# Kernel tuning notes

Measured on AMD Instinct MI355X. Metric: run time of the kernel, lower is better.

## Reference

```python
import jax, jax.numpy as jnp
import numpy as np

B, T, D = 4, 4096, 512
H, L = 8, 6
HD = D // H
BS = 64          # block_size
MLP = 2048
VOCAB = 96000
MAX_SCALE = 10000.0
LN_EPS = 1e-6


def _sinusoidal_pe(length, dim, max_scale=MAX_SCALE):
    # flax common_layers sinusoidal init (concat sin|cos halves)
    pos = np.arange(length)[:, None].astype(np.float32)
    div = np.exp(np.arange(0, dim, 2).astype(np.float32) * -(np.log(max_scale) / dim))
    pe = np.zeros((length, dim), dtype=np.float32)
    pe[:, : dim // 2] = np.sin(pos * div)
    pe[:, dim // 2:] = np.cos(pos * div)
    return jnp.asarray(pe)

_PE = _sinusoidal_pe(T, D)


def layer_norm(x, scale, bias):
    m = jnp.mean(x, axis=-1, keepdims=True)
    v = jnp.mean(jnp.square(x - m), axis=-1, keepdims=True)
    return (x - m) * jax.lax.rsqrt(v + LN_EPS) * scale + bias


def local_block_attention(x, mask, wq, wk, wv, wo, stagger):
    # x: [B, T, D], mask: [B, T] bool (True = real token)
    b, t, d = x.shape
    if stagger:
        lp = BS // 2
        rp = BS - lp
        x = jnp.pad(x, ((0, 0), (lp, rp), (0, 0)))
        mask = jnp.pad(mask, ((0, 0), (lp, rp)))
    tp = x.shape[1]
    nb = tp // BS
    xb = x.reshape(b, nb, BS, d)          # [B, nb, BS, D]
    mb = mask.reshape(b, nb, BS)          # [B, nb, BS]
    scale = 1.0 / float(np.sqrt(HD))
    q = jnp.einsum('bnsd,dhf->bnshf', xb, wq) * scale
    k = jnp.einsum('bnsd,dhf->bnshf', xb, wk)
    v = jnp.einsum('bnsd,dhf->bnshf', xb, wv)
    scores = jnp.einsum('bnqhf,bnkhf->bnhqk', q, k)       # [B, nb, H, BS, BS]
    scores = jnp.where(mb[:, :, None, None, :], scores, jnp.asarray(-1e9, scores.dtype))
    probs = jax.nn.softmax(scores, axis=-1)
    o = jnp.einsum('bnhqk,bnkhf->bnqhf', probs, v)
    o = jnp.einsum('bnqhf,hfd->bnqd', o, wo).reshape(b, tp, d)
    if stagger:
        o = o[:, lp:lp + t]
    return o


def setup_inputs() -> dict:
    key = jax.random.key(0)
    ks = jax.random.split(key, 10)
    inputs = jax.random.randint(ks[0], (B, T), 0, VOCAB)
    embed = jax.random.normal(ks[1], (VOCAB, D), dtype=jnp.float32)
    s = 0.02
    wq = jax.random.normal(ks[2], (L, D, H, HD), dtype=jnp.float32) * s
    wk = jax.random.normal(ks[3], (L, D, H, HD), dtype=jnp.float32) * s
    wv = jax.random.normal(ks[4], (L, D, H, HD), dtype=jnp.float32) * s
    wo = jax.random.normal(ks[5], (L, H, HD, D), dtype=jnp.float32) * s
    w1 = jax.random.normal(ks[6], (L, D, MLP), dtype=jnp.float32) * s
    b1 = jnp.zeros((L, MLP), dtype=jnp.float32)
    w2 = jax.random.normal(ks[7], (L, MLP, D), dtype=jnp.float32) * s
    b2 = jnp.zeros((L, D), dtype=jnp.float32)
    ln1_s = jnp.ones((L, D), dtype=jnp.float32)
    ln1_b = jnp.zeros((L, D), dtype=jnp.float32)
    ln2_s = jnp.ones((L, D), dtype=jnp.float32)
    ln2_b = jnp.zeros((L, D), dtype=jnp.float32)
    lnf_s = jnp.ones((D,), dtype=jnp.float32)
    lnf_b = jnp.zeros((D,), dtype=jnp.float32)
    return {'inputs': inputs, 'embed': embed, 'wq': wq, 'wk': wk, 'wv': wv, 'wo': wo,
            'ln1_s': ln1_s, 'ln1_b': ln1_b, 'ln2_s': ln2_s, 'ln2_b': ln2_b,
            'w1': w1, 'b1': b1, 'w2': w2, 'b2': b2, 'lnf_s': lnf_s, 'lnf_b': lnf_b}


def reference(inputs, embed, wq, wk, wv, wo, ln1_s, ln1_b, ln2_s, ln2_b,
              w1, b1, w2, b2, lnf_s, lnf_b):
    mask = inputs > 0                      # src padding mask [B, T]
    x = embed[inputs.astype(jnp.int32)]    # [B, T, D]
    x = x + _PE[None, :, :]                # sinusoidal position embedding
    for lyr in range(L):
        stagger = (lyr % 2 == 1)           # stagger_local_blocks on odd layers
        h = layer_norm(x, ln1_s[lyr], ln1_b[lyr])
        h = local_block_attention(h, mask, wq[lyr], wk[lyr], wv[lyr], wo[lyr], stagger)
        x = x + h
        y = layer_norm(x, ln2_s[lyr], ln2_b[lyr])
        y = jnp.matmul(jax.nn.relu(jnp.matmul(y, w1[lyr]) + b1[lyr]), w2[lyr]) + b2[lyr]
        x = x + y
    return layer_norm(x, lnf_s, lnf_b)
```

## Files before the change

kernel.cpp:

```cpp
#include <hip/hip_runtime.h>

typedef unsigned short u16;
typedef unsigned int   u32;
typedef __attribute__((ext_vector_type(8))) short short8;
typedef __attribute__((ext_vector_type(4))) float f32x4;

#define TSEQ   4096
#define DMODEL 512
#define NHEAD  8
#define HDIM   64
#define NLAYER 6
#define MLPD   2048

#define GPTR(p) (const __attribute__((address_space(1))) void*)(p)
#define LPTR(p) (__attribute__((address_space(3))) void*)(p)

__device__ __forceinline__ u16 f2b(float f) {
  u32 u = __float_as_uint(f);
  u32 r = (u + 0x7fffu + ((u >> 16) & 1u)) >> 16;
  return (u16)r;
}
__device__ __forceinline__ float b2f(u16 h) { return __uint_as_float(((u32)h) << 16); }

__device__ __forceinline__ short8 ld8g(const u16* p, bool ok) {
  if (ok) return *(const short8*)p;
  short8 z = {0, 0, 0, 0, 0, 0, 0, 0};
  return z;
}

__global__ __launch_bounds__(256) void transpose_convert_all(
    const float* __restrict__ wq, const float* __restrict__ wk,
    const float* __restrict__ wv, const float* __restrict__ wo,
    const float* __restrict__ w1, const float* __restrict__ w2,
    u16* __restrict__ wqkv_bt, u16* __restrict__ wo_bt,
    u16* __restrict__ w1_bt, u16* __restrict__ w2_bt) {
  __shared__ float tile[64][65];
  int bx = blockIdx.x, l = blockIdx.y;
  const float* W; u16* out; int K, N, Ntot, ro, kb, nb2;
  if (bx < 256) {
    int which = bx >> 6, local = bx & 63;
    K = 512; N = 512; kb = local & 7; nb2 = local >> 3;
    if (which == 0)      { W = wq; out = wqkv_bt; Ntot = 1536; ro = 0; }
    else if (which == 1) { W = wk; out = wqkv_bt; Ntot = 1536; ro = 512; }
    else if (which == 2) { W = wv; out = wqkv_bt; Ntot = 1536; ro = 1024; }
    else                 { W = wo; out = wo_bt;   Ntot = 512;  ro = 0; }
  } else if (bx < 512) {
    int local = bx - 256;
    W = w1; out = w1_bt; K = 512; N = 2048; Ntot = 2048; ro = 0;
    kb = local & 7; nb2 = local >> 3;
  } else {
    int local = bx - 512;
    W = w2; out = w2_bt; K = 2048; N = 512; Ntot = 512; ro = 0;
    kb = local >> 3; nb2 = local & 7;
  }
  int k0 = kb * 64, n0 = nb2 * 64;
  const float* Wl = W + (size_t)l * K * N;
  u16* Ol = out + (size_t)l * Ntot * K;
  int tx = threadIdx.x & 15, ty = threadIdx.x >> 4;
#pragma unroll
  for (int p = 0; p < 4; ++p) {
    int k = k0 + p * 16 + ty;
    float4 v = *(const float4*)(Wl + (size_t)k * N + n0 + tx * 4);
    tile[p * 16 + ty][tx * 4 + 0] = v.x;
    tile[p * 16 + ty][tx * 4 + 1] = v.y;
    tile[p * 16 + ty][tx * 4 + 2] = v.z;
    tile[p * 16 + ty][tx * 4 + 3] = v.w;
  }
  __syncthreads();
#pragma unroll
  for (int p = 0; p < 4; ++p) {
    int n = n0 + p * 16 + ty;
    ushort4 s;
    s.x = f2b(tile[tx * 4 + 0][p * 16 + ty]);
    s.y = f2b(tile[tx * 4 + 1][p * 16 + ty]);
    s.z = f2b(tile[tx * 4 + 2][p * 16 + ty]);
    s.w = f2b(tile[tx * 4 + 3][p * 16 + ty]);
    *(ushort4*)(Ol + (size_t)(ro + n) * K + k0 + tx * 4) = s;
  }
}

__global__ void embed_pe_kernel(const int* __restrict__ idx,
                                const float* __restrict__ embed,
                                float* __restrict__ x) {
  int i = blockIdx.x;
  int t = i & (TSEQ - 1);
  int tok = idx[i];
  int c = threadIdx.x * 4;
  float4 e = *(const float4*)(embed + (size_t)tok * DMODEL + c);
  float vals[4] = {e.x, e.y, e.z, e.w};
  float o[4];
#pragma unroll
  for (int j = 0; j < 4; ++j) {
    int col = c + j;
    int jj = (col < 256) ? col : col - 256;
    float div = __expf((float)jj * -0.035977892078032f);
    float arg = (float)t * div;
    o[j] = vals[j] + ((col < 256) ? __sinf(arg) : __cosf(arg));
  }
  float4 r = {o[0], o[1], o[2], o[3]};
  *(float4*)(x + (size_t)i * DMODEL + c) = r;
}

template <bool OUT_BF16>
__global__ __launch_bounds__(256) void ln_kernel(
    const float* __restrict__ x, const float* __restrict__ gamma,
    const float* __restrict__ beta, void* __restrict__ out) {
  int wave = threadIdx.x >> 6, lane = threadIdx.x & 63;
  int row = (blockIdx.x << 2) + wave;
  const float* xr = x + (size_t)row * DMODEL + lane * 8;
  float4 a = *(const float4*)xr;
  float4 b = *(const float4*)(xr + 4);
  float v[8] = {a.x, a.y, a.z, a.w, b.x, b.y, b.z, b.w};
  float s = 0.f;
#pragma unroll
  for (int j = 0; j < 8; ++j) s += v[j];
#pragma unroll
  for (int off = 1; off < 64; off <<= 1) s += __shfl_xor(s, off, 64);
  float mean = s * (1.0f / 512.0f);
  float q = 0.f;
#pragma unroll
  for (int j = 0; j < 8; ++j) { float d = v[j] - mean; q += d * d; }
#pragma unroll
  for (int off = 1; off < 64; off <<= 1) q += __shfl_xor(q, off, 64);
  float rstd = rsqrtf(q * (1.0f / 512.0f) + 1e-6f);
  float4 g0 = *(const float4*)(gamma + lane * 8);
  float4 g1 = *(const float4*)(gamma + lane * 8 + 4);
  float4 p0 = *(const float4*)(beta + lane * 8);
  float4 p1 = *(const float4*)(beta + lane * 8 + 4);
  float g[8] = {g0.x, g0.y, g0.z, g0.w, g1.x, g1.y, g1.z, g1.w};
  float be[8] = {p0.x, p0.y, p0.z, p0.w, p1.x, p1.y, p1.z, p1.w};
  float r[8];
#pragma unroll
  for (int j = 0; j < 8; ++j) r[j] = (v[j] - mean) * rstd * g[j] + be[j];
  if (OUT_BF16) {
    uint4 pk;
    pk.x = (u32)f2b(r[0]) | ((u32)f2b(r[1]) << 16);
    pk.y = (u32)f2b(r[2]) | ((u32)f2b(r[3]) << 16);
    pk.z = (u32)f2b(r[4]) | ((u32)f2b(r[5]) << 16);
    pk.w = (u32)f2b(r[6]) | ((u32)f2b(r[7]) << 16);
    *(uint4*)((u16*)out + (size_t)row * DMODEL + lane * 8) = pk;
  } else {
    float4 r0 = {r[0], r[1], r[2], r[3]};
    float4 r1 = {r[4], r[5], r[6], r[7]};
    float* op = (float*)out + (size_t)row * DMODEL + lane * 8;
    *(float4*)op = r0;
    *(float4*)(op + 4) = r1;
  }
}

template <int FLAGS>
__global__ __launch_bounds__(256) void gemm_kernel(
    const u16* __restrict__ A, const u16* __restrict__ Bt,
    const float* __restrict__ bias, const float* __restrict__ resid,
    void* __restrict__ out, void* __restrict__ out2, int M, int N, int K) {
  __shared__ __align__(16) u16 a_lds[3][128][32];
  __shared__ __align__(16) u16 b_lds[3][128][32];
  int m0 = blockIdx.y * 128, n0 = blockIdx.x * 128;
  int t = threadIdx.x;
  int lr = t >> 2, lc = (t & 3) * 8;
  int wave = t >> 6, lane = t & 63;
  int wm = (wave >> 1) * 64, wn = (wave & 1) * 64;
  int fr = lane & 15, quad = lane >> 4;

  f32x4 acc[4][4];
  f32x4 zz = {0.f, 0.f, 0.f, 0.f};
#pragma unroll
  for (int i = 0; i < 4; ++i)
#pragma unroll
    for (int j = 0; j < 4; ++j) acc[i][j] = zz;

  const u16* Ag0 = A + (size_t)(m0 + lr) * K + lc;
  const u16* Ag1 = A + (size_t)(m0 + lr + 64) * K + lc;
  const u16* Bg0 = Bt + (size_t)(n0 + lr) * K + lc;
  const u16* Bg1 = Bt + (size_t)(n0 + lr + 64) * K + lc;

  __builtin_amdgcn_global_load_lds(GPTR(Ag0), LPTR(&a_lds[0][lr][lc]), 16, 0, 0);
  __builtin_amdgcn_global_load_lds(GPTR(Ag1), LPTR(&a_lds[0][lr + 64][lc]), 16, 0, 0);
  __builtin_amdgcn_global_load_lds(GPTR(Bg0), LPTR(&b_lds[0][lr][lc]), 16, 0, 0);
  __builtin_amdgcn_global_load_lds(GPTR(Bg1), LPTR(&b_lds[0][lr + 64][lc]), 16, 0, 0);

  int T = K >> 5;
  int buf = 0;
  for (int tt = 0; tt < T; ++tt) {
    int nb = buf + 1 == 3 ? 0 : buf + 1;
    if (tt + 1 < T) {
      int off = (tt + 1) << 5;
      __builtin_amdgcn_global_load_lds(GPTR(Ag0 + off), LPTR(&a_lds[nb][lr][lc]), 16, 0, 0);
      __builtin_amdgcn_global_load_lds(GPTR(Ag1 + off), LPTR(&a_lds[nb][lr + 64][lc]), 16, 0, 0);
      __builtin_amdgcn_global_load_lds(GPTR(Bg0 + off), LPTR(&b_lds[nb][lr][lc]), 16, 0, 0);
      __builtin_amdgcn_global_load_lds(GPTR(Bg1 + off), LPTR(&b_lds[nb][lr + 64][lc]), 16, 0, 0);
      asm volatile("s_waitcnt vmcnt(4)\n\ts_barrier" ::: "memory");
    } else {
      asm volatile("s_waitcnt vmcnt(0)\n\ts_barrier" ::: "memory");
    }
    short8 af[4], bf[4];
#pragma unroll
    for (int mi = 0; mi < 4; ++mi)
      af[mi] = *(const short8*)&a_lds[buf][wm + mi * 16 + fr][quad * 8];
#pragma unroll
    for (int ni = 0; ni < 4; ++ni)
      bf[ni] = *(const short8*)&b_lds[buf][wn + ni * 16 + fr][quad * 8];
#pragma unroll
    for (int mi = 0; mi < 4; ++mi)
#pragma unroll
      for (int ni = 0; ni < 4; ++ni)
        acc[mi][ni] = __builtin_amdgcn_mfma_f32_16x16x32_bf16(
            af[mi], bf[ni], acc[mi][ni], 0, 0, 0);
    buf = nb;
  }

  if (FLAGS & 16) {
#pragma unroll
    for (int mi = 0; mi < 4; ++mi)
#pragma unroll
      for (int ni = 0; ni < 4; ++ni) {
        int colg = n0 + wn + ni * 16 + fr;
        if (colg < 1024) {
#pragma unroll
          for (int r = 0; r < 4; ++r) {
            int rowg = m0 + wm + mi * 16 + quad * 4 + r;
            ((u16*)out)[(size_t)rowg * 1024 + colg] = f2b(acc[mi][ni][r]);
          }
        } else {
          int hh = (colg - 1024) >> 6, ff = colg & 63;
          int rowg0 = m0 + wm + mi * 16 + quad * 4;
          int bb = rowg0 >> 12, tok = rowg0 & 4095;
          ushort4 pk;
          pk.x = f2b(acc[mi][ni][0]);
          pk.y = f2b(acc[mi][ni][1]);
          pk.z = f2b(acc[mi][ni][2]);
          pk.w = f2b(acc[mi][ni][3]);
          *(ushort4*)((u16*)out2 +
                      ((size_t)(bb * 8 + hh) * 64 + ff) * 4096 + tok) = pk;
        }
      }
    return;
  }

#pragma unroll
  for (int mi = 0; mi < 4; ++mi)
#pragma unroll
    for (int ni = 0; ni < 4; ++ni) {
      int colg = n0 + wn + ni * 16 + fr;
      float bv = (FLAGS & 1) ? bias[colg] : 0.0f;
#pragma unroll
      for (int r = 0; r < 4; ++r) {
        int rowg = m0 + wm + mi * 16 + quad * 4 + r;
        float val = acc[mi][ni][r] + bv;
        if (FLAGS & 2) val = fmaxf(val, 0.0f);
        if (FLAGS & 4) val += resid[(size_t)rowg * N + colg];
        if (FLAGS & 8)
          ((u16*)out)[(size_t)rowg * N + colg] = f2b(val);
        else
          ((float*)out)[(size_t)rowg * N + colg] = val;
      }
    }
}

template <int FLAGS>
__global__ __launch_bounds__(512, 2) void gemm256_kernel(
    const u16* __restrict__ A, const u16* __restrict__ Bt,
    const float* __restrict__ bias, const float* __restrict__ resid,
    void* __restrict__ out, void* __restrict__ out2, int M, int N, int K) {
  __shared__ __align__(16) u16 a_lds[2][16384];
  __shared__ __align__(16) u16 b_lds[2][16384];
  int m0 = blockIdx.y * 256, n0 = blockIdx.x * 256;
  int tid = threadIdx.x;
  int w = tid >> 6, lane = tid & 63;
  int fr = lane & 15, quad = lane >> 4;
  int wms = (w >> 2) * 8;
  int wns = (w & 3) * 4;
  int rS = lane >> 2;
  int cS = ((lane & 3) * 8) ^ ((lane & 32) ? 16 : 0);
  const u16* Asrc = A + (size_t)(m0 + w * 16 + rS) * K + cS;
  const u16* Bsrc = Bt + (size_t)(n0 + w * 16 + rS) * K + cS;
  int wBase = w * 1024 + lane * 8;
  int rdoff = fr * 32 + ((quad * 8) ^ ((fr & 8) ? 16 : 0));
  int NT = K >> 6;

  f32x4 acc[8][4];
  f32x4 zz = {0.f, 0.f, 0.f, 0.f};
#pragma unroll
  for (int i = 0; i < 8; ++i)
#pragma unroll
    for (int j = 0; j < 4; ++j) acc[i][j] = zz;

  auto stage_half = [&](int hh) {
    if (hh >= 4 * NT) return;
    int th = hh >> 2, part = hh & 3, kk = part >> 1;
    const u16* src = (part & 1) ? Bsrc : Asrc;
    u16* ldsb = (part & 1) ? &b_lds[0][0] : &a_lds[0][0];
    ldsb += (size_t)(th & 1) * 16384;
    src += (size_t)th * 64 + kk * 32;
#pragma unroll
    for (int j = 0; j < 2; ++j) {
      __builtin_amdgcn_global_load_lds(GPTR(src + (size_t)j * 128 * K),
                                       LPTR(ldsb + kk * 512 + j * 8192 + wBase),
                                       16, 0, 0);
    }
  };

#pragma unroll
  for (int hh = 0; hh < 6; ++hh) stage_half(hh);
  asm volatile("s_waitcnt vmcnt(4)\n\ts_barrier" ::: "memory");

  for (int t = 0; t < NT; ++t) {
    const u16* ap = a_lds[t & 1];
    const u16* bp = b_lds[t & 1];
    short8 aF[4], bF[4];
#define LDA256(mi_, kk_) (*(const short8*)&ap[((wms + (mi_)) * 2 + (kk_)) * 512 + rdoff])
#define LDB256(ni_, kk_) (*(const short8*)&bp[((wns + (ni_)) * 2 + (kk_)) * 512 + rdoff])
#pragma unroll
    for (int ni = 0; ni < 4; ++ni) bF[ni] = LDB256(ni, 0);
#pragma unroll
    for (int mi = 0; mi < 4; ++mi) aF[mi] = LDA256(mi, 0);
    stage_half(4 * t + 6);
    __builtin_amdgcn_s_barrier();
    __builtin_amdgcn_s_setprio(1);
#pragma unroll
    for (int mi = 0; mi < 4; ++mi)
#pragma unroll
      for (int ni = 0; ni < 4; ++ni)
        acc[mi][ni] = __builtin_amdgcn_mfma_f32_16x16x32_bf16(
            aF[mi], bF[ni], acc[mi][ni], 0, 0, 0);
    __builtin_amdgcn_s_setprio(0);
    __builtin_amdgcn_s_barrier();
#pragma unroll
    for (int mi = 0; mi < 4; ++mi) aF[mi] = LDA256(4 + mi, 0);
    stage_half(4 * t + 7);
    __builtin_amdgcn_s_barrier();
    __builtin_amdgcn_s_setprio(1);
#pragma unroll
    for (int mi = 0; mi < 4; ++mi)
#pragma unroll
      for (int ni = 0; ni < 4; ++ni)
        acc[4 + mi][ni] = __builtin_amdgcn_mfma_f32_16x16x32_bf16(
            aF[mi], bF[ni], acc[4 + mi][ni], 0, 0, 0);
    __builtin_amdgcn_s_setprio(0);
    __builtin_amdgcn_s_barrier();
#pragma unroll
    for (int ni = 0; ni < 4; ++ni) bF[ni] = LDB256(ni, 1);
#pragma unroll
    for (int mi = 0; mi < 4; ++mi) aF[mi] = LDA256(mi, 1);
    stage_half(4 * t + 8);
    __builtin_amdgcn_s_barrier();
    __builtin_amdgcn_s_setprio(1);
#pragma unroll
    for (int mi = 0; mi < 4; ++mi)
#pragma unroll
      for (int ni = 0; ni < 4; ++ni)
        acc[mi][ni] = __builtin_amdgcn_mfma_f32_16x16x32_bf16(
            aF[mi], bF[ni], acc[mi][ni], 0, 0, 0);
    __builtin_amdgcn_s_setprio(0);
    __builtin_amdgcn_s_barrier();
#pragma unroll
    for (int mi = 0; mi < 4; ++mi) aF[mi] = LDA256(4 + mi, 1);
    stage_half(4 * t + 9);
    __builtin_amdgcn_s_barrier();
    __builtin_amdgcn_s_setprio(1);
#pragma unroll
    for (int mi = 0; mi < 4; ++mi)
#pragma unroll
      for (int ni = 0; ni < 4; ++ni)
        acc[4 + mi][ni] = __builtin_amdgcn_mfma_f32_16x16x32_bf16(
            aF[mi], bF[ni], acc[4 + mi][ni], 0, 0, 0);
    __builtin_amdgcn_s_setprio(0);
    if (t + 2 == NT)
      asm volatile("s_waitcnt vmcnt(0)\n\ts_barrier" ::: "memory");
    else if (t + 1 < NT)
      asm volatile("s_waitcnt vmcnt(4)\n\ts_barrier" ::: "memory");
#undef LDA256
#undef LDB256
  }

  int wm = (w >> 2) * 128, wn = (w & 3) * 64;
  if (FLAGS & 16) {
#pragma unroll
    for (int mi = 0; mi < 8; ++mi)
#pragma unroll
      for (int ni = 0; ni < 4; ++ni) {
        int colg = n0 + wn + ni * 16 + fr;
        if (colg < 1024) {
#pragma unroll
          for (int r = 0; r < 4; ++r) {
            int rowg = m0 + wm + mi * 16 + quad * 4 + r;
            ((u16*)out)[(size_t)rowg * 1024 + colg] = f2b(acc[mi][ni][r]);
          }
        } else {
          int hh = (colg - 1024) >> 6, ff = colg & 63;
          int rowg0 = m0 + wm + mi * 16 + quad * 4;
          int bb2 = rowg0 >> 12, tok = rowg0 & 4095;
          ushort4 pk;
          pk.x = f2b(acc[mi][ni][0]);
          pk.y = f2b(acc[mi][ni][1]);
          pk.z = f2b(acc[mi][ni][2]);
          pk.w = f2b(acc[mi][ni][3]);
          *(ushort4*)((u16*)out2 +
                      ((size_t)(bb2 * 8 + hh) * 64 + ff) * 4096 + tok) = pk;
        }
      }
    return;
  }

#pragma unroll
  for (int mi = 0; mi < 8; ++mi)
#pragma unroll
    for (int ni = 0; ni < 4; ++ni) {
      int colg = n0 + wn + ni * 16 + fr;
      float bv = (FLAGS & 1) ? bias[colg] : 0.0f;
#pragma unroll
      for (int r = 0; r < 4; ++r) {
        int rowg = m0 + wm + mi * 16 + quad * 4 + r;
        float val = acc[mi][ni][r] + bv;
        if (FLAGS & 2) val = fmaxf(val, 0.0f);
        if (FLAGS & 4) val += resid[(size_t)rowg * N + colg];
        if (FLAGS & 8)
          ((u16*)out)[(size_t)rowg * N + colg] = f2b(val);
        else
          ((float*)out)[(size_t)rowg * N + colg] = val;
      }
    }
}

__global__ __launch_bounds__(128) void attn_mfma_kernel(
    const u16* __restrict__ qk, const u16* __restrict__ vt,
    const int* __restrict__ tokens, u16* __restrict__ o, int sh) {
  __shared__ __align__(16) u16 ps[2][64][72];
  __shared__ float kmask[64];
  int n = blockIdx.x, hg = blockIdx.y, b = blockIdx.z;
  int tid = threadIdx.x;
  int w = tid >> 6, lane = tid & 63;
  int head = hg * 2 + w;
  int fr = lane & 15, quad = lane >> 4;

  if (tid < 64) {
    int pp = n * 64 + tid - sh;
    kmask[tid] =
        (pp >= 0 && pp < TSEQ && tokens[(size_t)b * TSEQ + pp] > 0) ? 1.f : 0.f;
  }
  __syncthreads();

  const u16* qkb = qk + (size_t)b * TSEQ * 1024;

  f32x4 st[4][4];
  f32x4 zz = {0.f, 0.f, 0.f, 0.f};
#pragma unroll
  for (int i = 0; i < 4; ++i)
#pragma unroll
    for (int j = 0; j < 4; ++j) st[i][j] = zz;
#pragma unroll
  for (int kk = 0; kk < 2; ++kk) {
    short8 ka[4], qb[4];
#pragma unroll
    for (int mi = 0; mi < 4; ++mi) {
      int p = n * 64 + mi * 16 + fr - sh;
      ka[mi] = ld8g(qkb + (ptrdiff_t)p * 1024 + 512 + head * 64 + kk * 32 + quad * 8,
                    p >= 0 && p < TSEQ);
    }
#pragma unroll
    for (int ni = 0; ni < 4; ++ni) {
      int p = n * 64 + ni * 16 + fr - sh;
      qb[ni] = ld8g(qkb + (ptrdiff_t)p * 1024 + head * 64 + kk * 32 + quad * 8,
                    p >= 0 && p < TSEQ);
    }
#pragma unroll
    for (int mi = 0; mi < 4; ++mi)
#pragma unroll
      for (int ni = 0; ni < 4; ++ni)
        st[mi][ni] = __builtin_amdgcn_mfma_f32_16x16x32_bf16(
            ka[mi], qb[ni], st[mi][ni], 0, 0, 0);
  }

  float kmv[4][4];
#pragma unroll
  for (int mi = 0; mi < 4; ++mi)
#pragma unroll
    for (int r = 0; r < 4; ++r) kmv[mi][r] = kmask[mi * 16 + quad * 4 + r];
#pragma unroll
  for (int ni = 0; ni < 4; ++ni) {
    float mx = -3.0e38f;
#pragma unroll
    for (int mi = 0; mi < 4; ++mi)
#pragma unroll
      for (int r = 0; r < 4; ++r) {
        float s = (kmv[mi][r] > 0.f) ? st[mi][ni][r] * 0.125f : -1.0e9f;
        st[mi][ni][r] = s;
        mx = fmaxf(mx, s);
      }
    mx = fmaxf(mx, __shfl_xor(mx, 16, 64));
    mx = fmaxf(mx, __shfl_xor(mx, 32, 64));
    float sm = 0.f;
#pragma unroll
    for (int mi = 0; mi < 4; ++mi)
#pragma unroll
      for (int r = 0; r < 4; ++r) {
        float e = __expf(st[mi][ni][r] - mx);
        st[mi][ni][r] = e;
        sm += e;
      }
    sm += __shfl_xor(sm, 16, 64);
    sm += __shfl_xor(sm, 32, 64);
    float inv = 1.0f / sm;
#pragma unroll
    for (int mi = 0; mi < 4; ++mi)
#pragma unroll
      for (int r = 0; r < 4; ++r) st[mi][ni][r] *= inv;
  }

#pragma unroll
  for (int mi = 0; mi < 4; ++mi)
#pragma unroll
    for (int ni = 0; ni < 4; ++ni) {
      uint2 pk;
      pk.x = (u32)f2b(st[mi][ni][0]) | ((u32)f2b(st[mi][ni][1]) << 16);
      pk.y = (u32)f2b(st[mi][ni][2]) | ((u32)f2b(st[mi][ni][3]) << 16);
      *(uint2*)&ps[w][ni * 16 + fr][mi * 16 + quad * 4] = pk;
    }
  __syncthreads();

  f32x4 oc[4][4];
#pragma unroll
  for (int i = 0; i < 4; ++i)
#pragma unroll
    for (int j = 0; j < 4; ++j) oc[i][j] = zz;
  const u16* vtb = vt + (size_t)(b * 8 + head) * 64 * 4096;
#pragma unroll
  for (int kk = 0; kk < 2; ++kk) {
    short8 pa[4], vb[4];
#pragma unroll
    for (int mi = 0; mi < 4; ++mi)
      pa[mi] = *(const short8*)&ps[w][mi * 16 + fr][kk * 32 + quad * 8];
    int key0 = n * 64 - sh + kk * 32 + quad * 8;
    bool kok = (key0 >= 0) && (key0 < TSEQ);
#pragma unroll
    for (int ni = 0; ni < 4; ++ni)
      vb[ni] = ld8g(vtb + (size_t)(ni * 16 + fr) * 4096 + key0, kok);
#pragma unroll
    for (int mi = 0; mi < 4; ++mi)
#pragma unroll
      for (int ni = 0; ni < 4; ++ni)
        oc[mi][ni] = __builtin_amdgcn_mfma_f32_16x16x32_bf16(
            pa[mi], vb[ni], oc[mi][ni], 0, 0, 0);
  }

#pragma unroll
  for (int mi = 0; mi < 4; ++mi)
#pragma unroll
    for (int ni = 0; ni < 4; ++ni)
#pragma unroll
      for (int r = 0; r < 4; ++r) {
        int q = mi * 16 + quad * 4 + r;
        int p = n * 64 + q - sh;
        if (p >= 0 && p < TSEQ)
          o[((size_t)(b * TSEQ + p)) * DMODEL + head * 64 + ni * 16 + fr] =
              f2b(oc[mi][ni][r]);
      }
}

extern "C" void kernel_launch(void* const* d_in, const int* in_sizes, int n_in,
                              void* d_out, int out_size, void* d_ws, size_t ws_size,
                              hipStream_t stream) {
  (void)in_sizes; (void)n_in; (void)out_size; (void)ws_size;
  const int*   tokens = (const int*)d_in[0];
  const float* embed  = (const float*)d_in[1];
  const float* wq = (const float*)d_in[2];
  const float* wk = (const float*)d_in[3];
  const float* wv = (const float*)d_in[4];
  const float* wo = (const float*)d_in[5];
  const float* ln1_s = (const float*)d_in[6];
  const float* ln1_b = (const float*)d_in[7];
  const float* ln2_s = (const float*)d_in[8];
  const float* ln2_b = (const float*)d_in[9];
  const float* w1 = (const float*)d_in[10];
  const float* b1 = (const float*)d_in[11];
  const float* w2 = (const float*)d_in[12];
  const float* b2 = (const float*)d_in[13];
  const float* lnf_s = (const float*)d_in[14];
  const float* lnf_b = (const float*)d_in[15];

  char* ws = (char*)d_ws;
  const size_t MB = 1024ull * 1024ull;
  float* x     = (float*)(ws + 0);
  u16* h       = (u16*)(ws + 32 * MB);
  u16* qk      = (u16*)(ws + 48 * MB);
  u16* vt      = (u16*)(ws + 82 * MB);
  u16* obuf    = (u16*)(ws + 99 * MB);
  u16* hidden  = (u16*)(ws + 48 * MB);
  u16* wqkv_bt = (u16*)(ws + 116 * MB);
  u16* wo_bt   = (u16*)(ws + 126 * MB);
  u16* w1_bt   = (u16*)(ws + 130 * MB);
  u16* w2_bt   = (u16*)(ws + 143 * MB);

  transpose_convert_all<<<dim3(768, 6), 256, 0, stream>>>(
      wq, wk, wv, wo, w1, w2, wqkv_bt, wo_bt, w1_bt, w2_bt);

  embed_pe_kernel<<<16384, 128, 0, stream>>>(tokens, embed, x);

  for (int l = 0; l < NLAYER; ++l) {
    int sh = (l & 1) ? 32 : 0;
    int nb = (l & 1) ? 65 : 64;
    ln_kernel<true><<<4096, 256, 0, stream>>>(x, ln1_s + l * 512, ln1_b + l * 512, h);
    gemm256_kernel<16><<<dim3(6, 64), 512, 0, stream>>>(
        h, wqkv_bt + (size_t)l * 1536 * 512, nullptr, nullptr, qk, vt,
        16384, 1536, 512);
    attn_mfma_kernel<<<dim3(nb, 4, 4), 128, 0, stream>>>(qk, vt, tokens, obuf, sh);
    gemm_kernel<4><<<dim3(4, 128), 256, 0, stream>>>(
        obuf, wo_bt + (size_t)l * 512 * 512, nullptr, x, x, nullptr,
        16384, 512, 512);
    ln_kernel<true><<<4096, 256, 0, stream>>>(x, ln2_s + l * 512, ln2_b + l * 512, h);
    gemm256_kernel<1 | 2 | 8><<<dim3(8, 64), 512, 0, stream>>>(
        h, w1_bt + (size_t)l * 2048 * 512, b1 + l * 2048, nullptr, hidden, nullptr,
        16384, 2048, 512);
    gemm_kernel<1 | 4><<<dim3(4, 128), 256, 0, stream>>>(
        hidden, w2_bt + (size_t)l * 512 * 2048, b2 + l * 512, x, x, nullptr,
        16384, 512, 2048);
  }
  ln_kernel<false><<<4096, 256, 0, stream>>>(x, lnf_s, lnf_b, d_out);
}
```

Measured before the change: 1.600 ms.

## Replace 128x128 GEMM with pipelined 256x128 tile kernel for N=512 GEMMs

Adds a 256x128-tile, 512-thread GEMM kernel that reuses the swizzled LDS layout, double buffering and staged prefetch of the 256x256 kernel, with setprio around MFMA bursts. It replaces the older 128x128 triple-buffered kernel for the attention output projection and the MLP down projection. The aim is more data reuse per tile and better overlap of loads with MFMA. The grid halves to 256 blocks, which leaves fewer blocks per CU on a 256-CU part and may reduce occupancy.

```diff
diff --git a/kernel.cpp b/kernel.cpp
--- a/kernel.cpp
+++ b/kernel.cpp
@@ -149,115 +149,6 @@
 }
 
 template <int FLAGS>
-__global__ __launch_bounds__(256) void gemm_kernel(
-    const u16* __restrict__ A, const u16* __restrict__ Bt,
-    const float* __restrict__ bias, const float* __restrict__ resid,
-    void* __restrict__ out, void* __restrict__ out2, int M, int N, int K) {
-  __shared__ __align__(16) u16 a_lds[3][128][32];
-  __shared__ __align__(16) u16 b_lds[3][128][32];
-  int m0 = blockIdx.y * 128, n0 = blockIdx.x * 128;
-  int t = threadIdx.x;
-  int lr = t >> 2, lc = (t & 3) * 8;
-  int wave = t >> 6, lane = t & 63;
-  int wm = (wave >> 1) * 64, wn = (wave & 1) * 64;
-  int fr = lane & 15, quad = lane >> 4;
-
-  f32x4 acc[4][4];
-  f32x4 zz = {0.f, 0.f, 0.f, 0.f};
-#pragma unroll
-  for (int i = 0; i < 4; ++i)
-#pragma unroll
-    for (int j = 0; j < 4; ++j) acc[i][j] = zz;
-
-  const u16* Ag0 = A + (size_t)(m0 + lr) * K + lc;
-  const u16* Ag1 = A + (size_t)(m0 + lr + 64) * K + lc;
-  const u16* Bg0 = Bt + (size_t)(n0 + lr) * K + lc;
-  const u16* Bg1 = Bt + (size_t)(n0 + lr + 64) * K + lc;
-
-  __builtin_amdgcn_global_load_lds(GPTR(Ag0), LPTR(&a_lds[0][lr][lc]), 16, 0, 0);
-  __builtin_amdgcn_global_load_lds(GPTR(Ag1), LPTR(&a_lds[0][lr + 64][lc]), 16, 0, 0);
-  __builtin_amdgcn_global_load_lds(GPTR(Bg0), LPTR(&b_lds[0][lr][lc]), 16, 0, 0);
-  __builtin_amdgcn_global_load_lds(GPTR(Bg1), LPTR(&b_lds[0][lr + 64][lc]), 16, 0, 0);
-
-  int T = K >> 5;
-  int buf = 0;
-  for (int tt = 0; tt < T; ++tt) {
-    int nb = buf + 1 == 3 ? 0 : buf + 1;
-    if (tt + 1 < T) {
-      int off = (tt + 1) << 5;
-      __builtin_amdgcn_global_load_lds(GPTR(Ag0 + off), LPTR(&a_lds[nb][lr][lc]), 16, 0, 0);
-      __builtin_amdgcn_global_load_lds(GPTR(Ag1 + off), LPTR(&a_lds[nb][lr + 64][lc]), 16, 0, 0);
-      __builtin_amdgcn_global_load_lds(GPTR(Bg0 + off), LPTR(&b_lds[nb][lr][lc]), 16, 0, 0);
-      __builtin_amdgcn_global_load_lds(GPTR(Bg1 + off), LPTR(&b_lds[nb][lr + 64][lc]), 16, 0, 0);
-      asm volatile("s_waitcnt vmcnt(4)\n\ts_barrier" ::: "memory");
-    } else {
-      asm volatile("s_waitcnt vmcnt(0)\n\ts_barrier" ::: "memory");
-    }
-    short8 af[4], bf[4];
-#pragma unroll
-    for (int mi = 0; mi < 4; ++mi)
-      af[mi] = *(const short8*)&a_lds[buf][wm + mi * 16 + fr][quad * 8];
-#pragma unroll
-    for (int ni = 0; ni < 4; ++ni)
-      bf[ni] = *(const short8*)&b_lds[buf][wn + ni * 16 + fr][quad * 8];
-#pragma unroll
-    for (int mi = 0; mi < 4; ++mi)
-#pragma unroll
-      for (int ni = 0; ni < 4; ++ni)
-        acc[mi][ni] = __builtin_amdgcn_mfma_f32_16x16x32_bf16(
-            af[mi], bf[ni], acc[mi][ni], 0, 0, 0);
-    buf = nb;
-  }
-
-  if (FLAGS & 16) {
-#pragma unroll
-    for (int mi = 0; mi < 4; ++mi)
-#pragma unroll
-      for (int ni = 0; ni < 4; ++ni) {
-        int colg = n0 + wn + ni * 16 + fr;
-        if (colg < 1024) {
-#pragma unroll
-          for (int r = 0; r < 4; ++r) {
-            int rowg = m0 + wm + mi * 16 + quad * 4 + r;
-            ((u16*)out)[(size_t)rowg * 1024 + colg] = f2b(acc[mi][ni][r]);
-          }
-        } else {
-          int hh = (colg - 1024) >> 6, ff = colg & 63;
-          int rowg0 = m0 + wm + mi * 16 + quad * 4;
-          int bb = rowg0 >> 12, tok = rowg0 & 4095;
-          ushort4 pk;
-          pk.x = f2b(acc[mi][ni][0]);
-          pk.y = f2b(acc[mi][ni][1]);
-          pk.z = f2b(acc[mi][ni][2]);
-          pk.w = f2b(acc[mi][ni][3]);
-          *(ushort4*)((u16*)out2 +
-                      ((size_t)(bb * 8 + hh) * 64 + ff) * 4096 + tok) = pk;
-        }
-      }
-    return;
-  }
-
-#pragma unroll
-  for (int mi = 0; mi < 4; ++mi)
-#pragma unroll
-    for (int ni = 0; ni < 4; ++ni) {
-      int colg = n0 + wn + ni * 16 + fr;
-      float bv = (FLAGS & 1) ? bias[colg] : 0.0f;
-#pragma unroll
-      for (int r = 0; r < 4; ++r) {
-        int rowg = m0 + wm + mi * 16 + quad * 4 + r;
-        float val = acc[mi][ni][r] + bv;
-        if (FLAGS & 2) val = fmaxf(val, 0.0f);
-        if (FLAGS & 4) val += resid[(size_t)rowg * N + colg];
-        if (FLAGS & 8)
-          ((u16*)out)[(size_t)rowg * N + colg] = f2b(val);
-        else
-          ((float*)out)[(size_t)rowg * N + colg] = val;
-      }
-    }
-}
-
-template <int FLAGS>
 __global__ __launch_bounds__(512, 2) void gemm256_kernel(
     const u16* __restrict__ A, const u16* __restrict__ Bt,
     const float* __restrict__ bias, const float* __restrict__ resid,
@@ -404,6 +295,144 @@
 
 #pragma unroll
   for (int mi = 0; mi < 8; ++mi)
+#pragma unroll
+    for (int ni = 0; ni < 4; ++ni) {
+      int colg = n0 + wn + ni * 16 + fr;
+      float bv = (FLAGS & 1) ? bias[colg] : 0.0f;
+#pragma unroll
+      for (int r = 0; r < 4; ++r) {
+        int rowg = m0 + wm + mi * 16 + quad * 4 + r;
+        float val = acc[mi][ni][r] + bv;
+        if (FLAGS & 2) val = fmaxf(val, 0.0f);
+        if (FLAGS & 4) val += resid[(size_t)rowg * N + colg];
+        if (FLAGS & 8)
+          ((u16*)out)[(size_t)rowg * N + colg] = f2b(val);
+        else
+          ((float*)out)[(size_t)rowg * N + colg] = val;
+      }
+    }
+}
+
+template <int FLAGS>
+__global__ __launch_bounds__(512, 2) void gemm256x128_kernel(
+    const u16* __restrict__ A, const u16* __restrict__ Bt,
+    const float* __restrict__ bias, const float* __restrict__ resid,
+    void* __restrict__ out, int M, int N, int K) {
+  __shared__ __align__(16) u16 a_lds[2][16384];
+  __shared__ __align__(16) u16 b_lds[2][8192];
+  int m0 = blockIdx.y * 256, n0 = blockIdx.x * 128;
+  int tid = threadIdx.x;
+  int w = tid >> 6, lane = tid & 63;
+  int fr = lane & 15, quad = lane >> 4;
+  int wms = (w >> 1) * 4;
+  int wns = (w & 1) * 4;
+  int rS = lane >> 2;
+  int cS = ((lane & 3) * 8) ^ ((lane & 32) ? 16 : 0);
+  const u16* Asrc = A + (size_t)(m0 + w * 16 + rS) * K + cS;
+  const u16* Bsrc = Bt + (size_t)(n0 + w * 16 + rS) * K + cS;
+  int wBase = w * 1024 + lane * 8;
+  int rdoff = fr * 32 + ((quad * 8) ^ ((fr & 8) ? 16 : 0));
+  int NT = K >> 6;
+
+  f32x4 acc[4][4];
+  f32x4 zz = {0.f, 0.f, 0.f, 0.f};
+#pragma unroll
+  for (int i = 0; i < 4; ++i)
+#pragma unroll
+    for (int j = 0; j < 4; ++j) acc[i][j] = zz;
+
+  auto stage_unit = [&](int g) {
+    if (g >= 4 * NT) return;
+    int th = g >> 2, part = g & 3, kk = part >> 1;
+    if (part & 1) {
+      const u16* src = Bsrc + (size_t)th * 64 + kk * 32;
+      u16* ldsb = &b_lds[th & 1][0];
+      __builtin_amdgcn_global_load_lds(GPTR(src), LPTR(ldsb + kk * 512 + wBase),
+                                       16, 0, 0);
+    } else {
+      const u16* src = Asrc + (size_t)th * 64 + kk * 32;
+      u16* ldsb = &a_lds[th & 1][0];
+#pragma unroll
+      for (int j = 0; j < 2; ++j) {
+        __builtin_amdgcn_global_load_lds(GPTR(src + (size_t)j * 128 * K),
+                                         LPTR(ldsb + kk * 512 + j * 8192 + wBase),
+                                         16, 0, 0);
+      }
+    }
+  };
+
+#pragma unroll
+  for (int g = 0; g < 6; ++g) stage_unit(g);
+  asm volatile("s_waitcnt vmcnt(3)\n\ts_barrier" ::: "memory");
+
+  for (int t = 0; t < NT; ++t) {
+    const u16* ap = a_lds[t & 1];
+    const u16* bp = b_lds[t & 1];
+    short8 bF[4], a0, a1;
+#define LDA(mi_, kk_) (*(const short8*)&ap[((wms + (mi_)) * 2 + (kk_)) * 512 + rdoff])
+#define LDB(ni_, kk_) (*(const short8*)&bp[((wns + (ni_)) * 2 + (kk_)) * 512 + rdoff])
+#pragma unroll
+    for (int ni = 0; ni < 4; ++ni) bF[ni] = LDB(ni, 0);
+    a0 = LDA(0, 0); a1 = LDA(1, 0);
+    stage_unit(4 * t + 6);
+    __builtin_amdgcn_s_barrier();
+    __builtin_amdgcn_s_setprio(1);
+#pragma unroll
+    for (int ni = 0; ni < 4; ++ni)
+      acc[0][ni] = __builtin_amdgcn_mfma_f32_16x16x32_bf16(a0, bF[ni], acc[0][ni], 0, 0, 0);
+#pragma unroll
+    for (int ni = 0; ni < 4; ++ni)
+      acc[1][ni] = __builtin_amdgcn_mfma_f32_16x16x32_bf16(a1, bF[ni], acc[1][ni], 0, 0, 0);
+    __builtin_amdgcn_s_setprio(0);
+    __builtin_amdgcn_s_barrier();
+    a0 = LDA(2, 0); a1 = LDA(3, 0);
+    stage_unit(4 * t + 7);
+    __builtin_amdgcn_s_barrier();
+    __builtin_amdgcn_s_setprio(1);
+#pragma unroll
+    for (int ni = 0; ni < 4; ++ni)
+      acc[2][ni] = __builtin_amdgcn_mfma_f32_16x16x32_bf16(a0, bF[ni], acc[2][ni], 0, 0, 0);
+#pragma unroll
+    for (int ni = 0; ni < 4; ++ni)
+      acc[3][ni] = __builtin_amdgcn_mfma_f32_16x16x32_bf16(a1, bF[ni], acc[3][ni], 0, 0, 0);
+    __builtin_amdgcn_s_setprio(0);
+    __builtin_amdgcn_s_barrier();
+#pragma unroll
+    for (int ni = 0; ni < 4; ++ni) bF[ni] = LDB(ni, 1);
+    a0 = LDA(0, 1); a1 = LDA(1, 1);
+    stage_unit(4 * t + 8);
+    __builtin_amdgcn_s_barrier();
+    __builtin_amdgcn_s_setprio(1);
+#pragma unroll
+    for (int ni = 0; ni < 4; ++ni)
+      acc[0][ni] = __builtin_amdgcn_mfma_f32_16x16x32_bf16(a0, bF[ni], acc[0][ni], 0, 0, 0);
+#pragma unroll
+    for (int ni = 0; ni < 4; ++ni)
+      acc[1][ni] = __builtin_amdgcn_mfma_f32_16x16x32_bf16(a1, bF[ni], acc[1][ni], 0, 0, 0);
+    __builtin_amdgcn_s_setprio(0);
+    __builtin_amdgcn_s_barrier();
+    a0 = LDA(2, 1); a1 = LDA(3, 1);
+    stage_unit(4 * t + 9);
+    __builtin_amdgcn_s_barrier();
+    __builtin_amdgcn_s_setprio(1);
+#pragma unroll
+    for (int ni = 0; ni < 4; ++ni)
+      acc[2][ni] = __builtin_amdgcn_mfma_f32_16x16x32_bf16(a0, bF[ni], acc[2][ni], 0, 0, 0);
+#pragma unroll
+    for (int ni = 0; ni < 4; ++ni)
+      acc[3][ni] = __builtin_amdgcn_mfma_f32_16x16x32_bf16(a1, bF[ni], acc[3][ni], 0, 0, 0);
+    __builtin_amdgcn_s_setprio(0);
+    if (t + 2 == NT)
+      asm volatile("s_waitcnt vmcnt(0)\n\ts_barrier" ::: "memory");
+    else if (t + 1 < NT)
+      asm volatile("s_waitcnt vmcnt(3)\n\ts_barrier" ::: "memory");
+#undef LDA
+#undef LDB
+  }
+
+  int wm = (w >> 1) * 64, wn = (w & 1) * 64;
+#pragma unroll
+  for (int mi = 0; mi < 4; ++mi)
 #pragma unroll
     for (int ni = 0; ni < 4; ++ni) {
       int colg = n0 + wn + ni * 16 + fr;
@@ -604,15 +633,15 @@
         h, wqkv_bt + (size_t)l * 1536 * 512, nullptr, nullptr, qk, vt,
         16384, 1536, 512);
     attn_mfma_kernel<<<dim3(nb, 4, 4), 128, 0, stream>>>(qk, vt, tokens, obuf, sh);
-    gemm_kernel<4><<<dim3(4, 128), 256, 0, stream>>>(
-        obuf, wo_bt + (size_t)l * 512 * 512, nullptr, x, x, nullptr,
+    gemm256x128_kernel<4><<<dim3(4, 64), 512, 0, stream>>>(
+        obuf, wo_bt + (size_t)l * 512 * 512, nullptr, x, x,
         16384, 512, 512);
     ln_kernel<true><<<4096, 256, 0, stream>>>(x, ln2_s + l * 512, ln2_b + l * 512, h);
     gemm256_kernel<1 | 2 | 8><<<dim3(8, 64), 512, 0, stream>>>(
         h, w1_bt + (size_t)l * 2048 * 512, b1 + l * 2048, nullptr, hidden, nullptr,
         16384, 2048, 512);
-    gemm_kernel<1 | 4><<<dim3(4, 128), 256, 0, stream>>>(
-        hidden, w2_bt + (size_t)l * 512 * 2048, b2 + l * 512, x, x, nullptr,
+    gemm256x128_kernel<1 | 4><<<dim3(4, 64), 512, 0, stream>>>(
+        hidden, w2_bt + (size_t)l * 512 * 2048, b2 + l * 512, x, x,
         16384, 512, 2048);
   }
   ln_kernel<false><<<4096, 256, 0, stream>>>(x, lnf_s, lnf_b, d_out);
```

After: 1.675 ms. 4.7% more time.
